# Optimization experiments

Measured on AMD Instinct MI355X. Metric: run time of the kernel, lower is better.

## Reference

```python
import jax, jax.numpy as jnp
import numpy as np

HIDDEN = 2048
NUM_HEADS = 16
HEAD_DIM = HIDDEN // NUM_HEADS


def setup_inputs() -> dict:
    key = jax.random.key(0)
    ks = jax.random.split(key, 10)
    B, S = 2, 2048
    scale = 1.0 / np.sqrt(HIDDEN)
    inp = {
        "x": jax.random.normal(ks[0], (B, S, HIDDEN), dtype=jnp.float32),
        "attention_mask": jnp.zeros((B, S), dtype=jnp.float32),
        "Wq": jax.random.normal(ks[1], (HIDDEN, HIDDEN), dtype=jnp.float32) * scale,
        "bq": jnp.zeros((HIDDEN,), dtype=jnp.float32),
        "Wk": jax.random.normal(ks[2], (HIDDEN, HIDDEN), dtype=jnp.float32) * scale,
        "bk": jnp.zeros((HIDDEN,), dtype=jnp.float32),
        "Wv": jax.random.normal(ks[3], (HIDDEN, HIDDEN), dtype=jnp.float32) * scale,
        "bv": jnp.zeros((HIDDEN,), dtype=jnp.float32),
        "Wo": jax.random.normal(ks[4], (HIDDEN, HIDDEN), dtype=jnp.float32) * scale,
        "bo": jnp.zeros((HIDDEN,), dtype=jnp.float32),
    }
    return inp


def _split_heads(t):
    # [B, S, H*D] -> [B, H, S, D]
    B, S, _ = t.shape
    return t.reshape(B, S, NUM_HEADS, HEAD_DIM).transpose(0, 2, 1, 3)


def reference(x, attention_mask, Wq, bq, Wk, bk, Wv, bv, Wo, bo):
    B, S, _ = x.shape
    # Linear layers: y = x @ W^T + b (torch nn.Linear convention)
    q = _split_heads(x @ Wq.T + bq)  # [B, H, S, D]
    k = _split_heads(x @ Wk.T + bk)
    v = _split_heads(x @ Wv.T + bv)
    scale = 1.0 / jnp.sqrt(jnp.asarray(HEAD_DIM, dtype=x.dtype))
    scores = jnp.einsum("bhqd,bhkd->bhqk", q, k) * scale  # [B, H, S, S]
    scores = scores + attention_mask[:, None, None, :]  # additive mask broadcast
    attn = jax.nn.softmax(scores, axis=-1)
    out = jnp.einsum("bhqk,bhkd->bhqd", attn, v)  # [B, H, S, D]
    out = out.transpose(0, 2, 1, 3).reshape(B, S, HIDDEN)
    return out @ Wo.T + bo
```

## Files before the change

kernel.cpp:

```cpp
#include <hip/hip_runtime.h>
#include <math.h>

constexpr int S_LEN = 2048;
constexpr int HID   = 2048;
constexpr int NH    = 16;
constexpr int HD    = 128;

typedef __attribute__((ext_vector_type(8))) short short8;
typedef __attribute__((ext_vector_type(4))) float floatx4;

static __device__ __forceinline__ ushort f2bf(float f) {
  union { float f; unsigned u; } v; v.f = f;
  unsigned r = (v.u + 0x7fffu + ((v.u >> 16) & 1u)) >> 16;
  return (ushort)r;
}
static __device__ __forceinline__ ushort f2bf_fast(float f) {
  union { float f; unsigned u; } v; v.f = f;
  return (ushort)((v.u + 0x8000u) >> 16);
}

static __device__ __forceinline__ void glds16(const ushort* g, ushort* l) {
  __builtin_amdgcn_global_load_lds(
      (const __attribute__((address_space(1))) void*)g,
      (__attribute__((address_space(3))) void*)l, 16, 0, 0);
}

static __device__ __forceinline__ void cvt4(ushort* dst, const float* src, size_t i) {
  const float4 v = ((const float4*)src)[i];
  ushort4 u = {f2bf(v.x), f2bf(v.y), f2bf(v.z), f2bf(v.w)};
  ((ushort4*)dst)[i] = u;
}

__global__ __launch_bounds__(256)
void convert_all(const float* __restrict__ x,
                 const float* __restrict__ wq, const float* __restrict__ wk,
                 const float* __restrict__ wv, const float* __restrict__ wo,
                 ushort* __restrict__ xb, ushort* __restrict__ wqb,
                 ushort* __restrict__ wkb, ushort* __restrict__ wvb,
                 ushort* __restrict__ wob) {
  const size_t gid = blockIdx.x * 256 + threadIdx.x;
  const size_t T = gridDim.x * 256;
  const size_t NX = (size_t)4096 * HID / 4;
  const size_t NW = (size_t)HID * HID / 4;
  for (size_t i = gid; i < NX; i += T) cvt4(xb, x, i);
  for (size_t i = gid; i < NW; i += T) {
    cvt4(wqb, wq, i);
    cvt4(wkb, wk, i);
    cvt4(wvb, wv, i);
    cvt4(wob, wo, i);
  }
}

template <bool BF16OUT>
__device__ __forceinline__
void gemm_core(const ushort* __restrict__ A, const ushort* __restrict__ W,
               const float* __restrict__ bias, void* __restrict__ Cv,
               int m0, int n0) {
  __shared__ __align__(16) ushort As[4096];
  __shared__ __align__(16) ushort Bs[4096];

  const int tid  = threadIdx.x;
  const int lane = tid & 63;
  const int w    = tid >> 6;
  const int wm   = w >> 1, wn = w & 1;
  const int n16  = lane & 15, q4 = lane >> 4;

  const int sr = lane >> 2;
  const int sc = (lane & 3) ^ ((lane >> 4) & 3);
  const ushort* ag0 = A + (size_t)(m0 + w*32 + sr) * HID + sc*8;
  const ushort* ag1 = ag0 + (size_t)16 * HID;
  const ushort* bg0 = W + (size_t)(n0 + w*32 + sr) * HID + sc*8;
  const ushort* bg1 = bg0 + (size_t)16 * HID;
  ushort* al0 = As + (w*2 + 0) * 512;
  ushort* al1 = As + (w*2 + 1) * 512;
  ushort* bl0 = Bs + (w*2 + 0) * 512;
  ushort* bl1 = Bs + (w*2 + 1) * 512;

  const int fp = n16*4 + (q4 ^ ((n16 >> 2) & 3));

  floatx4 acc[4][4];
  #pragma unroll
  for (int i = 0; i < 4; ++i)
    #pragma unroll
    for (int j = 0; j < 4; ++j) acc[i][j] = (floatx4)0.f;

  for (int kb0 = 0; kb0 < HID; kb0 += 32) {
    __syncthreads();
    glds16(ag0 + kb0, al0);
    glds16(ag1 + kb0, al1);
    glds16(bg0 + kb0, bl0);
    glds16(bg1 + kb0, bl1);
    __syncthreads();

    short8 af[4], bf[4];
    #pragma unroll
    for (int t = 0; t < 4; ++t) {
      af[t] = *(const short8*)&As[(wm*4 + t)*512 + fp*8];
      bf[t] = *(const short8*)&Bs[(wn*4 + t)*512 + fp*8];
    }
    #pragma unroll
    for (int mt = 0; mt < 4; ++mt)
      #pragma unroll
      for (int nt = 0; nt < 4; ++nt)
        acc[mt][nt] = __builtin_amdgcn_mfma_f32_16x16x32_bf16(af[mt], bf[nt], acc[mt][nt], 0, 0, 0);
  }

  float bv4[4];
  #pragma unroll
  for (int nt = 0; nt < 4; ++nt) bv4[nt] = bias[n0 + wn*64 + nt*16 + n16];
  #pragma unroll
  for (int mt = 0; mt < 4; ++mt)
    #pragma unroll
    for (int nt = 0; nt < 4; ++nt)
      #pragma unroll
      for (int r = 0; r < 4; ++r) {
        const int row = m0 + wm*64 + mt*16 + q4*4 + r;
        const int col = n0 + wn*64 + nt*16 + n16;
        if (BF16OUT)
          ((ushort*)Cv)[(size_t)row * HID + col] = f2bf(acc[mt][nt][r] + bv4[nt]);
        else
          ((float*)Cv)[(size_t)row * HID + col] = acc[mt][nt][r] + bv4[nt];
      }
}

__global__ __launch_bounds__(256)
void gemm_qkv(const ushort* __restrict__ xb,
              const ushort* __restrict__ wqb, const ushort* __restrict__ wkb,
              const ushort* __restrict__ wvb,
              const float* __restrict__ bq, const float* __restrict__ bk,
              const float* __restrict__ bv,
              ushort* __restrict__ qb, ushort* __restrict__ kb_, ushort* __restrict__ vb) {
  const ushort* W; const float* bias; ushort* C;
  if (blockIdx.z == 0)      { W = wqb; bias = bq; C = qb;  }
  else if (blockIdx.z == 1) { W = wkb; bias = bk; C = kb_; }
  else                      { W = wvb; bias = bv; C = vb;  }
  gemm_core<true>(xb, W, bias, C, blockIdx.y * 128, blockIdx.x * 128);
}

__global__ __launch_bounds__(256)
void gemm_o(const ushort* __restrict__ ao, const ushort* __restrict__ wob,
            const float* __restrict__ bo, float* __restrict__ out) {
  gemm_core<false>(ao, wob, bo, out, blockIdx.y * 128, blockIdx.x * 128);
}

__global__ __launch_bounds__(256, 2)
void attn_mfma(const ushort* __restrict__ qb, const ushort* __restrict__ kbuf,
               const ushort* __restrict__ vb, const float* __restrict__ mask,
               ushort* __restrict__ ao) {
  __shared__ __align__(16) ushort Ks[64 * 136];
  __shared__ __align__(16) ushort Vs[128 * 72];
  __shared__ __align__(16) ushort Ps[4 * 32 * 72];

  const int tid  = threadIdx.x;
  const int w    = tid >> 6;
  const int lane = tid & 63;
  const int n16  = lane & 15;
  const int q4   = lane >> 4;
  const int b  = blockIdx.y >> 4;
  const int h  = blockIdx.y & 15;
  const int q0 = blockIdx.x * 128;
  const float scale = 0.08838834764831845f;

  ushort* Pw = Ps + w * (32 * 72);

  short8 aq[2][4];
  #pragma unroll
  for (int mt = 0; mt < 2; ++mt) {
    const ushort* qrow = qb + (size_t)(b*S_LEN + q0 + w*32 + mt*16 + n16)*HID + h*HD;
    #pragma unroll
    for (int kc = 0; kc < 4; ++kc)
      aq[mt][kc] = *(const short8*)(qrow + kc*32 + q4*8);
  }

  floatx4 oacc[2][8];
  float lp[2][4];
  #pragma unroll
  for (int mt = 0; mt < 2; ++mt) {
    #pragma unroll
    for (int dt = 0; dt < 8; ++dt) oacc[mt][dt] = (floatx4)0.f;
    #pragma unroll
    for (int r = 0; r < 4; ++r) lp[mt][r] = 0.f;
  }

  const int srow = tid >> 2;
  const int sseg = (tid & 3) * 32;
  const ushort* kg = kbuf + (size_t)(b*S_LEN + srow)*HID + h*HD + sseg;
  const ushort* vg = vb   + (size_t)(b*S_LEN + srow)*HID + h*HD + sseg;

  uint4 kr[4], vr[4];
  #pragma unroll
  for (int j = 0; j < 4; ++j) {
    kr[j] = *(const uint4*)(kg + j*8);
    vr[j] = *(const uint4*)(vg + j*8);
  }

  for (int kb0 = 0; kb0 < S_LEN; kb0 += 64) {
    __syncthreads();
    #pragma unroll
    for (int j = 0; j < 4; ++j)
      *(uint4*)&Ks[srow*136 + sseg + j*8] = kr[j];
    const ushort* vsc = (const ushort*)vr;
    #pragma unroll
    for (int j = 0; j < 32; ++j)
      Vs[(sseg + j)*72 + srow] = vsc[j];
    if (kb0 + 64 < S_LEN) {
      const size_t ko = (size_t)64 * HID;
      const ushort* kg2 = kg + (size_t)(kb0 + 64) * HID;
      const ushort* vg2 = vg + (size_t)(kb0 + 64) * HID;
      #pragma unroll
      for (int j = 0; j < 4; ++j) {
        kr[j] = *(const uint4*)(kg2 + j*8);
        vr[j] = *(const uint4*)(vg2 + j*8);
      }
      (void)ko;
    }
    __syncthreads();

    floatx4 acc[2][4];
    #pragma unroll
    for (int mt = 0; mt < 2; ++mt)
      #pragma unroll
      for (int nt = 0; nt < 4; ++nt) acc[mt][nt] = (floatx4)0.f;
    #pragma unroll
    for (int nt = 0; nt < 4; ++nt) {
      #pragma unroll
      for (int kc = 0; kc < 4; ++kc) {
        const short8 bk = *(const short8*)&Ks[(nt*16 + n16)*136 + kc*32 + q4*8];
        acc[0][nt] = __builtin_amdgcn_mfma_f32_16x16x32_bf16(aq[0][kc], bk, acc[0][nt], 0, 0, 0);
        acc[1][nt] = __builtin_amdgcn_mfma_f32_16x16x32_bf16(aq[1][kc], bk, acc[1][nt], 0, 0, 0);
      }
    }

    float mk[4];
    #pragma unroll
    for (int nt = 0; nt < 4; ++nt)
      mk[nt] = mask[(size_t)b*S_LEN + kb0 + nt*16 + n16];

    #pragma unroll
    for (int mt = 0; mt < 2; ++mt)
      #pragma unroll
      for (int r = 0; r < 4; ++r) {
        float p[4];
        #pragma unroll
        for (int nt = 0; nt < 4; ++nt) p[nt] = __expf(acc[mt][nt][r] * scale + mk[nt]);
        lp[mt][r] += (p[0] + p[1]) + (p[2] + p[3]);
        #pragma unroll
        for (int nt = 0; nt < 4; ++nt)
          Pw[(mt*16 + q4*4 + r)*72 + nt*16 + n16] = f2bf_fast(p[nt]);
      }

    #pragma unroll
    for (int kc2 = 0; kc2 < 2; ++kc2) {
      const short8 ap0 = *(const short8*)&Pw[(0*16 + n16)*72 + kc2*32 + q4*8];
      const short8 ap1 = *(const short8*)&Pw[(1*16 + n16)*72 + kc2*32 + q4*8];
      #pragma unroll
      for (int dt = 0; dt < 8; ++dt) {
        const short8 bvf = *(const short8*)&Vs[(dt*16 + n16)*72 + kc2*32 + q4*8];
        oacc[0][dt] = __builtin_amdgcn_mfma_f32_16x16x32_bf16(ap0, bvf, oacc[0][dt], 0, 0, 0);
        oacc[1][dt] = __builtin_amdgcn_mfma_f32_16x16x32_bf16(ap1, bvf, oacc[1][dt], 0, 0, 0);
      }
    }
  }

  #pragma unroll
  for (int mt = 0; mt < 2; ++mt)
    #pragma unroll
    for (int r = 0; r < 4; ++r) {
      float l = lp[mt][r];
      l += __shfl_xor(l, 1);
      l += __shfl_xor(l, 2);
      l += __shfl_xor(l, 4);
      l += __shfl_xor(l, 8);
      lp[mt][r] = 1.0f / l;
    }

  #pragma unroll
  for (int mt = 0; mt < 2; ++mt)
    #pragma unroll
    for (int r = 0; r < 4; ++r) {
      const size_t rowoff = (size_t)(b*S_LEN + q0 + w*32 + mt*16 + q4*4 + r)*HID + h*HD;
      #pragma unroll
      for (int dt = 0; dt < 8; ++dt)
        ao[rowoff + dt*16 + n16] = f2bf(oacc[mt][dt][r] * lp[mt][r]);
    }
}

extern "C" void kernel_launch(void* const* d_in, const int* in_sizes, int n_in,
                              void* d_out, int out_size, void* d_ws, size_t ws_size,
                              hipStream_t stream) {
  (void)n_in; (void)out_size; (void)ws_size;
  const float* x    = (const float*)d_in[0];
  const float* mask = (const float*)d_in[1];
  const float* Wq   = (const float*)d_in[2];
  const float* bq   = (const float*)d_in[3];
  const float* Wk   = (const float*)d_in[4];
  const float* bk   = (const float*)d_in[5];
  const float* Wv   = (const float*)d_in[6];
  const float* bv   = (const float*)d_in[7];
  const float* Wo   = (const float*)d_in[8];
  const float* bo   = (const float*)d_in[9];
  float* out = (float*)d_out;

  const int B = in_sizes[0] / (S_LEN * HID);
  const int M = B * S_LEN;
  const size_t MH = (size_t)M * HID;
  const size_t WW = (size_t)HID * HID;

  ushort* xb   = (ushort*)d_ws;
  ushort* wqb  = xb   + MH;
  ushort* wkb  = wqb  + WW;
  ushort* wvb  = wkb  + WW;
  ushort* wob  = wvb  + WW;
  ushort* qb   = wob  + WW;
  ushort* kbuf = qb   + MH;
  ushort* vb   = kbuf + MH;
  ushort* ao   = xb;

  convert_all<<<512, 256, 0, stream>>>(x, Wq, Wk, Wv, Wo, xb, wqb, wkb, wvb, wob);
  gemm_qkv<<<dim3(HID/128, M/128, 3), 256, 0, stream>>>(xb, wqb, wkb, wvb, bq, bk, bv, qb, kbuf, vb);
  attn_mfma<<<dim3(S_LEN/128, B*NH), 256, 0, stream>>>(qb, kbuf, vb, mask, ao);
  gemm_o<<<dim3(HID/128, M/128), 256, 0, stream>>>(ao, wob, bo, out);
}
```

Measured before the change: 443.7 us.

## Pre-transpose V and stream K/V tiles into LDS via direct global-to-LDS loads

Adds a separate kernel that writes V in a per-head transposed [d, s] layout. The attention kernel can then load K and V tiles with global_load_lds using an XOR-swizzled LDS layout, replacing the register-staged prefetch and the scattered scalar V transpose stores. The output tile is also staged through LDS so it can be written to global memory as 16-byte stores. This costs an extra kernel launch and a full V read/write pass plus more workspace. It also drops the register prefetch overlap, so each tile load now sits between two barriers.

```diff
diff --git a/kernel.cpp b/kernel.cpp
--- a/kernel.cpp
+++ b/kernel.cpp
@@ -143,25 +143,52 @@
   gemm_core<false>(ao, wob, bo, out, blockIdx.y * 128, blockIdx.x * 128);
 }
 
+__global__ __launch_bounds__(256)
+void transpose_v(const ushort* __restrict__ vb, ushort* __restrict__ vt) {
+  __shared__ ushort T[64][72];
+  const int t  = threadIdx.x;
+  const int bh = blockIdx.z;
+  const int b = bh >> 4, h = bh & 15;
+  const int s0 = blockIdx.x * 64;
+  const int d0 = blockIdx.y * 64;
+  {
+    const int r = t >> 2, c = (t & 3) * 16;
+    const ushort* src = vb + (size_t)(b*S_LEN + s0 + r)*HID + h*HD + d0 + c;
+    *(uint4*)&T[r][c]     = *(const uint4*)src;
+    *(uint4*)&T[r][c + 8] = *(const uint4*)(src + 8);
+  }
+  __syncthreads();
+  {
+    const int dd = t >> 2, c = (t & 3) * 16;
+    ushort tmp[16];
+    #pragma unroll
+    for (int j = 0; j < 16; ++j) tmp[j] = T[c + j][dd];
+    ushort* dst = vt + (size_t)((b*NH + h)*HD + d0 + dd)*S_LEN + s0 + c;
+    *(uint4*)dst       = *(uint4*)tmp;
+    *(uint4*)(dst + 8) = *(uint4*)(tmp + 8);
+  }
+}
+
 __global__ __launch_bounds__(256, 2)
 void attn_mfma(const ushort* __restrict__ qb, const ushort* __restrict__ kbuf,
-               const ushort* __restrict__ vb, const float* __restrict__ mask,
+               const ushort* __restrict__ vtb, const float* __restrict__ mask,
                ushort* __restrict__ ao) {
-  __shared__ __align__(16) ushort Ks[64 * 136];
-  __shared__ __align__(16) ushort Vs[128 * 72];
-  __shared__ __align__(16) ushort Ps[4 * 32 * 72];
+  __shared__ __align__(16) ushort SM[25600];
 
   const int tid  = threadIdx.x;
   const int w    = tid >> 6;
   const int lane = tid & 63;
   const int n16  = lane & 15;
   const int q4   = lane >> 4;
+  const int n7   = n16 & 7;
   const int b  = blockIdx.y >> 4;
   const int h  = blockIdx.y & 15;
   const int q0 = blockIdx.x * 128;
   const float scale = 0.08838834764831845f;
 
-  ushort* Pw = Ps + w * (32 * 72);
+  ushort* Ks = SM;
+  ushort* Vs = SM + 8192;
+  ushort* Pw = SM + 16384 + w * 2304;
 
   short8 aq[2][4];
   #pragma unroll
@@ -172,6 +199,19 @@
       aq[mt][kc] = *(const short8*)(qrow + kc*32 + q4*8);
   }
 
+  const ushort* ksrc[4];
+  const ushort* vsrc[4];
+  #pragma unroll
+  for (int i = 0; i < 4; ++i) {
+    const int p = (w*4 + i)*64 + lane;
+    { const int rho = p >> 4, pc = p & 15;
+      const int cl = (pc & 8) | ((pc ^ rho) & 7);
+      ksrc[i] = kbuf + (size_t)(b*S_LEN + rho)*HID + h*HD + cl*8; }
+    { const int rho = p >> 3, pc = p & 7;
+      const int cl = (pc ^ rho) & 7;
+      vsrc[i] = vtb + ((size_t)(b*NH + h)*HD + rho)*S_LEN + cl*8; }
+  }
+
   floatx4 oacc[2][8];
   float lp[2][4];
   #pragma unroll
@@ -182,37 +222,12 @@
     for (int r = 0; r < 4; ++r) lp[mt][r] = 0.f;
   }
 
-  const int srow = tid >> 2;
-  const int sseg = (tid & 3) * 32;
-  const ushort* kg = kbuf + (size_t)(b*S_LEN + srow)*HID + h*HD + sseg;
-  const ushort* vg = vb   + (size_t)(b*S_LEN + srow)*HID + h*HD + sseg;
-
-  uint4 kr[4], vr[4];
-  #pragma unroll
-  for (int j = 0; j < 4; ++j) {
-    kr[j] = *(const uint4*)(kg + j*8);
-    vr[j] = *(const uint4*)(vg + j*8);
-  }
-
   for (int kb0 = 0; kb0 < S_LEN; kb0 += 64) {
     __syncthreads();
     #pragma unroll
-    for (int j = 0; j < 4; ++j)
-      *(uint4*)&Ks[srow*136 + sseg + j*8] = kr[j];
-    const ushort* vsc = (const ushort*)vr;
-    #pragma unroll
-    for (int j = 0; j < 32; ++j)
-      Vs[(sseg + j)*72 + srow] = vsc[j];
-    if (kb0 + 64 < S_LEN) {
-      const size_t ko = (size_t)64 * HID;
-      const ushort* kg2 = kg + (size_t)(kb0 + 64) * HID;
-      const ushort* vg2 = vg + (size_t)(kb0 + 64) * HID;
-      #pragma unroll
-      for (int j = 0; j < 4; ++j) {
-        kr[j] = *(const uint4*)(kg2 + j*8);
-        vr[j] = *(const uint4*)(vg2 + j*8);
-      }
-      (void)ko;
+    for (int i = 0; i < 4; ++i) {
+      glds16(ksrc[i] + (size_t)kb0 * HID, Ks + (w*4 + i)*512);
+      glds16(vsrc[i] + kb0,               Vs + (w*4 + i)*512);
     }
     __syncthreads();
 
@@ -225,7 +240,9 @@
     for (int nt = 0; nt < 4; ++nt) {
       #pragma unroll
       for (int kc = 0; kc < 4; ++kc) {
-        const short8 bk = *(const short8*)&Ks[(nt*16 + n16)*136 + kc*32 + q4*8];
+        const int cl = kc*4 + q4;
+        const int pc = (cl & 8) | ((cl ^ n7) & 7);
+        const short8 bk = *(const short8*)&Ks[(nt*16 + n16)*128 + pc*8];
         acc[0][nt] = __builtin_amdgcn_mfma_f32_16x16x32_bf16(aq[0][kc], bk, acc[0][nt], 0, 0, 0);
         acc[1][nt] = __builtin_amdgcn_mfma_f32_16x16x32_bf16(aq[1][kc], bk, acc[1][nt], 0, 0, 0);
       }
@@ -253,9 +270,11 @@
     for (int kc2 = 0; kc2 < 2; ++kc2) {
       const short8 ap0 = *(const short8*)&Pw[(0*16 + n16)*72 + kc2*32 + q4*8];
       const short8 ap1 = *(const short8*)&Pw[(1*16 + n16)*72 + kc2*32 + q4*8];
+      const int clb = kc2*4 + q4;
+      const int pcb = (clb ^ n7) & 7;
       #pragma unroll
       for (int dt = 0; dt < 8; ++dt) {
-        const short8 bvf = *(const short8*)&Vs[(dt*16 + n16)*72 + kc2*32 + q4*8];
+        const short8 bvf = *(const short8*)&Vs[(dt*16 + n16)*64 + pcb*8];
         oacc[0][dt] = __builtin_amdgcn_mfma_f32_16x16x32_bf16(ap0, bvf, oacc[0][dt], 0, 0, 0);
         oacc[1][dt] = __builtin_amdgcn_mfma_f32_16x16x32_bf16(ap1, bvf, oacc[1][dt], 0, 0, 0);
       }
@@ -274,15 +293,22 @@
       lp[mt][r] = 1.0f / l;
     }
 
+  __syncthreads();
+  ushort* dump = SM + w * 4352;
   #pragma unroll
   for (int mt = 0; mt < 2; ++mt)
     #pragma unroll
     for (int r = 0; r < 4; ++r) {
-      const size_t rowoff = (size_t)(b*S_LEN + q0 + w*32 + mt*16 + q4*4 + r)*HID + h*HD;
+      const int row = mt*16 + q4*4 + r;
       #pragma unroll
       for (int dt = 0; dt < 8; ++dt)
-        ao[rowoff + dt*16 + n16] = f2bf(oacc[mt][dt][r] * lp[mt][r]);
-    }
+        dump[row*136 + dt*16 + n16] = f2bf(oacc[mt][dt][r] * lp[mt][r]);
+    }
+  const int drow = lane >> 1, dhalf = lane & 1;
+  const size_t gbase = (size_t)(b*S_LEN + q0 + w*32 + drow)*HID + h*HD + dhalf*64;
+  #pragma unroll
+  for (int j = 0; j < 8; ++j)
+    *(uint4*)&ao[gbase + j*8] = *(const uint4*)&dump[drow*136 + dhalf*64 + j*8];
 }
 
 extern "C" void kernel_launch(void* const* d_in, const int* in_sizes, int n_in,
@@ -314,10 +340,12 @@
   ushort* qb   = wob  + WW;
   ushort* kbuf = qb   + MH;
   ushort* vb   = kbuf + MH;
+  ushort* vt   = vb   + MH;
   ushort* ao   = xb;
 
   convert_all<<<512, 256, 0, stream>>>(x, Wq, Wk, Wv, Wo, xb, wqb, wkb, wvb, wob);
   gemm_qkv<<<dim3(HID/128, M/128, 3), 256, 0, stream>>>(xb, wqb, wkb, wvb, bq, bk, bv, qb, kbuf, vb);
-  attn_mfma<<<dim3(S_LEN/128, B*NH), 256, 0, stream>>>(qb, kbuf, vb, mask, ao);
+  transpose_v<<<dim3(S_LEN/64, HD/64, B*NH), 256, 0, stream>>>(vb, vt);
+  attn_mfma<<<dim3(S_LEN/128, B*NH), 256, 0, stream>>>(qb, kbuf, vt, mask, ao);
   gemm_o<<<dim3(HID/128, M/128), 256, 0, stream>>>(ao, wob, bo, out);
 }
```

New measurement: 416.6 us. -6.1%, faster.
